# Kernel tuning notes

Measured on AMD Instinct MI355X. Metric: run time of the kernel, lower is better.

The kernel has to match this reference:

```python
import jax, jax.numpy as jnp
import numpy as np

N = 100000      # nodes
R = 8           # relations
E_DIM = 128     # embedding dim
N_EDGES = 1600000  # n * avg_degree(16)


def setup_inputs() -> dict:
    key = jax.random.key(0)
    k1, k2, k3, k4, k5 = jax.random.split(key, 5)
    x = jax.random.normal(k1, (N, E_DIM), dtype=jnp.float32)
    # xavier-ish scale for (r, e, e) relation weights
    weights = jax.random.normal(k2, (R, E_DIM, E_DIM), dtype=jnp.float32) * (1.0 / np.sqrt(E_DIM))
    edge_rel = jax.random.randint(k3, (N_EDGES,), 0, R, dtype=jnp.int32)
    edge_src = jax.random.randint(k4, (N_EDGES,), 0, N, dtype=jnp.int32)
    edge_dst = jax.random.randint(k5, (N_EDGES,), 0, N, dtype=jnp.int32)
    return dict(x=x, weights=weights, edge_rel=edge_rel, edge_src=edge_src, edge_dst=edge_dst)


def reference(x, weights, edge_rel, edge_src, edge_dst):
    n, e = x.shape
    r = weights.shape[0]
    # sparse adjacency row index: relation-block row = rel * n + dst  (shape rn)
    rows = edge_rel.astype(jnp.int32) * n + edge_dst.astype(jnp.int32)
    # row-normalized values: vals = 1 / row_degree (util.sum_sparse)
    deg = jax.ops.segment_sum(jnp.ones(rows.shape, dtype=x.dtype), rows, num_segments=r * n)
    vals = 1.0 / deg[rows]  # only evaluated at rows with >=1 edge
    # SpMM: h = graph @ x, viewed as (r, n, e)
    msgs = vals[:, None] * x[edge_src]                       # (E, e) gather
    h = jax.ops.segment_sum(msgs, rows, num_segments=r * n)  # (r*n, e) scatter-add
    h = h.reshape(r, n, e)
    # per-relation transform: (r, e_out, e_in) x (r, n, e_in) -> (n, r, e_out)
    h = jnp.einsum('rih,rnh->nri', weights, h)
    # SumUnify: relu(sum over relations)
    return jax.nn.relu(h.sum(axis=1))
```

## Files before the change

### kernel.cpp

```cpp
#include <hip/hip_runtime.h>
#include <hip/hip_bf16.h>

#define ED 128
#define RR 8
#define KTOT (RR * ED)
#define LDB 136

typedef __attribute__((ext_vector_type(8))) short short8;
typedef __attribute__((ext_vector_type(4))) float f32x4;

__device__ __forceinline__ unsigned short f2bf(float f){
  unsigned int u = __builtin_bit_cast(unsigned int, f);
  return (unsigned short)((u + 0x7fffu + ((u >> 16) & 1u)) >> 16);
}
__device__ __forceinline__ float bf2f(unsigned int lo){
  return __builtin_bit_cast(float, lo << 16);
}

__global__ void cast_bf16_vec(const float4* __restrict__ in, ushort4* __restrict__ out, int n4){
  int stride = gridDim.x * blockDim.x;
  for (int i = blockIdx.x * blockDim.x + threadIdx.x; i < n4; i += stride){
    float4 v = in[i];
    ushort4 o;
    o.x = f2bf(v.x); o.y = f2bf(v.y); o.z = f2bf(v.z); o.w = f2bf(v.w);
    out[i] = o;
  }
}

__global__ void hist_rank(const int* __restrict__ rel, const int* __restrict__ dst,
                          int* __restrict__ rowcnt, int* __restrict__ rank, int E){
  int stride = gridDim.x * blockDim.x;
  for (int i = blockIdx.x * blockDim.x + threadIdx.x; i < E; i += stride)
    rank[i] = atomicAdd(&rowcnt[(dst[i] << 3) | rel[i]], 1);
}

__launch_bounds__(1024)
__global__ void scan_block_sum(const int* __restrict__ rowcnt, int* __restrict__ bsum, int m){
  __shared__ int lds[16];
  int t = threadIdx.x;
  int idx = blockIdx.x * 1024 + t;
  int v = (idx < m) ? rowcnt[idx] : 0;
#pragma unroll
  for (int o = 32; o > 0; o >>= 1) v += __shfl_down(v, o);
  if ((t & 63) == 0) lds[t >> 6] = v;
  __syncthreads();
  if (t == 0){
    int s = 0;
#pragma unroll
    for (int w = 0; w < 16; ++w) s += lds[w];
    bsum[blockIdx.x] = s;
  }
}

__launch_bounds__(1024)
__global__ void scan_bsum_par(const int* __restrict__ bsum, int* __restrict__ bscan,
                              int nb, int* __restrict__ total_out){
  __shared__ int wsum[16];
  int t = threadIdx.x, lane = t & 63, wid = t >> 6;
  int v = (t < nb) ? bsum[t] : 0;
  int incl = v;
#pragma unroll
  for (int o = 1; o < 64; o <<= 1){
    int u = __shfl_up(incl, o);
    if (lane >= o) incl += u;
  }
  if (lane == 63) wsum[wid] = incl;
  __syncthreads();
  int woff = 0;
  for (int w0 = 0; w0 < wid; ++w0) woff += wsum[w0];
  if (t < nb) bscan[t] = woff + incl - v;
  if (t == nb - 1) *total_out = woff + incl;
}

__launch_bounds__(1024)
__global__ void scan_final(const int* __restrict__ rowcnt, const int* __restrict__ bscan,
                           int* __restrict__ row_ptr, int m){
  __shared__ int wsum[16];
  int t = threadIdx.x, lane = t & 63, wid = t >> 6;
  int idx = blockIdx.x * 1024 + t;
  int v = (idx < m) ? rowcnt[idx] : 0;
  int incl = v;
#pragma unroll
  for (int o = 1; o < 64; o <<= 1){
    int u = __shfl_up(incl, o);
    if (lane >= o) incl += u;
  }
  if (lane == 63) wsum[wid] = incl;
  __syncthreads();
  int woff = bscan[blockIdx.x];
  for (int w0 = 0; w0 < wid; ++w0) woff += wsum[w0];
  if (idx < m) row_ptr[idx] = woff + incl - v;
}

__global__ void scatter_pos(const int* __restrict__ rel, const int* __restrict__ src,
                            const int* __restrict__ dst, const int* __restrict__ rank,
                            const int* __restrict__ row_ptr, int* __restrict__ payload, int E){
  int stride = gridDim.x * blockDim.x;
  for (int i = blockIdx.x * blockDim.x + threadIdx.x; i < E; i += stride){
    int key = (dst[i] << 3) | rel[i];
    payload[row_ptr[key] + rank[i]] = src[i];
  }
}

__launch_bounds__(256)
__global__ void row_agg(const unsigned short* __restrict__ xb,
                        const int* __restrict__ row_ptr8,
                        const int* __restrict__ payload,
                        unsigned short* __restrict__ h2, int n){
  int d = (blockIdx.x * 256 + threadIdx.x) >> 6;
  int lane = threadIdx.x & 63;
  if (d >= n) return;
  int p9 = 0;
  if (lane < 9) p9 = row_ptr8[(d << 3) + lane];
  int base = __builtin_amdgcn_readlane(p9, 0);
  int pl = payload[base + lane];
  int win = 0;
  unsigned int* hp = (unsigned int*)h2 + ((size_t)d << 9) + lane;
#pragma unroll
  for (int r = 0; r < RR; ++r){
    int beg = __builtin_amdgcn_readlane(p9, r);
    int end = __builtin_amdgcn_readlane(p9, r + 1);
    float ax = 0.f, ay = 0.f;
    for (int e = beg; e < end; ++e){
      int idx = e - base;
      if ((idx >> 6) != win){
        win = idx >> 6;
        pl = payload[base + (win << 6) + lane];
      }
      int s = __builtin_amdgcn_readlane(pl, idx & 63);
      unsigned int v = ((const unsigned int*)(xb + ((size_t)s << 7)))[lane];
      ax += bf2f(v & 0xffffu);
      ay += bf2f(v >> 16);
    }
    float sc = (end > beg) ? 1.f / (float)(end - beg) : 0.f;
    hp[r << 6] = ((unsigned int)f2bf(ay * sc) << 16) | f2bf(ax * sc);
  }
}

__launch_bounds__(256)
__global__ void gemm_out(const unsigned short* __restrict__ h2,
                         const unsigned short* __restrict__ wbb,
                         float* __restrict__ out, int n){
  __shared__ __align__(16) unsigned short lds_a[128 * LDB];
  __shared__ __align__(16) unsigned short lds_b[128 * LDB];
  const int t = threadIdx.x;
  const int wave = t >> 6, lane = t & 63;
  const int wr = wave >> 1, wc = wave & 1;
  const int dbase = blockIdx.x * 128;
  const int frow = lane & 15, kb = lane >> 4;

  f32x4 acc[4][4];
#pragma unroll
  for (int rt = 0; rt < 4; ++rt)
#pragma unroll
    for (int jt = 0; jt < 4; ++jt)
      acc[rt][jt] = (f32x4){0.f, 0.f, 0.f, 0.f};

  for (int r = 0; r < RR; ++r){
    __syncthreads();
#pragma unroll
    for (int p = 0; p < 8; ++p){
      int q = p * 256 + t;
      int row = q >> 4, col = q & 15;
      int gr = dbase + row; if (gr >= n) gr = n - 1;
      *(short8*)&lds_a[row * LDB + col * 8] =
          *(const short8*)(h2 + (size_t)gr * KTOT + r * ED + col * 8);
    }
    const unsigned short* wp = wbb + (size_t)r * ED * ED;
#pragma unroll
    for (int p = 0; p < 8; ++p){
      int q = p * 256 + t;
      int row = q >> 4, col = q & 15;
      *(short8*)&lds_b[row * LDB + col * 8] = *(const short8*)(wp + row * ED + col * 8);
    }
    __syncthreads();

    short8 a[4][4], b[4][4];
#pragma unroll
    for (int rt = 0; rt < 4; ++rt)
#pragma unroll
      for (int ks = 0; ks < 4; ++ks)
        a[rt][ks] = *(const short8*)&lds_a[(wr * 64 + rt * 16 + frow) * LDB + ks * 32 + kb * 8];
#pragma unroll
    for (int jt = 0; jt < 4; ++jt)
#pragma unroll
      for (int ks = 0; ks < 4; ++ks)
        b[jt][ks] = *(const short8*)&lds_b[(wc * 64 + jt * 16 + frow) * LDB + ks * 32 + kb * 8];
#pragma unroll
    for (int rt = 0; rt < 4; ++rt)
#pragma unroll
      for (int jt = 0; jt < 4; ++jt)
#pragma unroll
        for (int ks = 0; ks < 4; ++ks)
          acc[rt][jt] = __builtin_amdgcn_mfma_f32_16x16x32_bf16(a[rt][ks], b[jt][ks], acc[rt][jt], 0, 0, 0);
  }

  const int drow = (lane >> 4) * 4;
  const int dcol = lane & 15;
#pragma unroll
  for (int rt = 0; rt < 4; ++rt)
#pragma unroll
    for (int jt = 0; jt < 4; ++jt)
#pragma unroll
      for (int reg = 0; reg < 4; ++reg){
        int i = dbase + wr * 64 + rt * 16 + drow + reg;
        if (i < n)
          out[(size_t)i * ED + wc * 64 + jt * 16 + dcol] = fmaxf(acc[rt][jt][reg], 0.f);
      }
}

extern "C" void kernel_launch(void* const* d_in, const int* in_sizes, int n_in,
                              void* d_out, int out_size, void* d_ws, size_t ws_size,
                              hipStream_t stream){
  const float* x  = (const float*)d_in[0];
  const float* w  = (const float*)d_in[1];
  const int* erel = (const int*)d_in[2];
  const int* esrc = (const int*)d_in[3];
  const int* edst = (const int*)d_in[4];
  float* out = (float*)d_out;

  const int n = in_sizes[0] / ED;
  const int E = in_sizes[2];
  const int m = n * RR;
  const int NB = (m + 1023) / 1024;

  char* ws = (char*)d_ws;
  size_t off = 0;
  auto alloc = [&](size_t bytes) -> char* {
    char* p = ws + off;
    off += (bytes + 255) & ~(size_t)255;
    return p;
  };
  unsigned short* h2      = (unsigned short*)alloc((size_t)n * KTOT * 2);
  unsigned short* xb      = (unsigned short*)alloc((size_t)n * ED * 2);
  unsigned short* wbb     = (unsigned short*)alloc((size_t)RR * ED * ED * 2);
  int*            payload = (int*)alloc((size_t)E * 4);
  int*            row_ptr = (int*)alloc((size_t)(m + 1) * 4);
  int*            rowcnt  = (int*)alloc((size_t)m * 4);
  int*            rank    = (int*)alloc((size_t)E * 4);
  int*            bsum    = (int*)alloc((size_t)NB * 4);
  int*            bscan   = (int*)alloc((size_t)NB * 4);
  if (off > ws_size || NB > 1024) return;

  hipMemsetAsync(rowcnt, 0, (size_t)m * 4, stream);

  cast_bf16_vec<<<2048, 256, 0, stream>>>((const float4*)x, (ushort4*)xb, n * ED / 4);
  cast_bf16_vec<<<128, 256, 0, stream>>>((const float4*)w, (ushort4*)wbb, RR * ED * ED / 4);
  hist_rank    <<<2048, 256, 0, stream>>>(erel, edst, rowcnt, rank, E);
  scan_block_sum<<<NB, 1024, 0, stream>>>(rowcnt, bsum, m);
  scan_bsum_par<<<1, 1024, 0, stream>>>(bsum, bscan, NB, row_ptr + m);
  scan_final   <<<NB, 1024, 0, stream>>>(rowcnt, bscan, row_ptr, m);
  scatter_pos  <<<2048, 256, 0, stream>>>(erel, esrc, edst, rank, row_ptr, payload, E);
  row_agg      <<<(n + 3) / 4, 256, 0, stream>>>(xb, row_ptr, payload, h2, n);
  gemm_out     <<<(n + 127) / 128, 256, 0, stream>>>(h2, wbb, out, n);
}
```

Baseline: 336.1 us.

## Split row aggregation across four waves per node and unroll gathers by four

The row aggregation kernel now assigns four wavefronts per destination node, each handling two relations, rather than one wave doing all eight. Within a wave the edge loop issues up to four independent row gathers per iteration to raise memory-level parallelism, with a fallback path for segments longer than 64 edges. This targets latency-bound gather throughput but launches four times as many waves and duplicates row-pointer loads.

Result: faster. 319.2 us (-5.0%).

```diff
diff --git a/kernel.cpp b/kernel.cpp
--- a/kernel.cpp
+++ b/kernel.cpp
@@ -107,33 +107,69 @@
                         const int* __restrict__ row_ptr8,
                         const int* __restrict__ payload,
                         unsigned short* __restrict__ h2, int n){
-  int d = (blockIdx.x * 256 + threadIdx.x) >> 6;
+  int wv   = (blockIdx.x * 256 + threadIdx.x) >> 6;
   int lane = threadIdx.x & 63;
+  int d    = wv >> 2;
+  int half = wv & 3;
   if (d >= n) return;
-  int p9 = 0;
-  if (lane < 9) p9 = row_ptr8[(d << 3) + lane];
-  int base = __builtin_amdgcn_readlane(p9, 0);
-  int pl = payload[base + lane];
-  int win = 0;
-  unsigned int* hp = (unsigned int*)h2 + ((size_t)d << 9) + lane;
-#pragma unroll
-  for (int r = 0; r < RR; ++r){
-    int beg = __builtin_amdgcn_readlane(p9, r);
-    int end = __builtin_amdgcn_readlane(p9, r + 1);
-    float ax = 0.f, ay = 0.f;
-    for (int e = beg; e < end; ++e){
-      int idx = e - base;
-      if ((idx >> 6) != win){
-        win = idx >> 6;
-        pl = payload[base + (win << 6) + lane];
+
+  int p3 = 0;
+  if (lane < 3) p3 = row_ptr8[(d << 3) + (half << 1) + lane];
+  int b0 = __builtin_amdgcn_readlane(p3, 0);
+  int b1 = __builtin_amdgcn_readlane(p3, 1);
+  int b2 = __builtin_amdgcn_readlane(p3, 2);
+  unsigned int* hp = (unsigned int*)h2 + ((size_t)d << 9) + ((size_t)half << 7) + lane;
+
+  if (b2 - b0 <= 64){
+    int pl = payload[b0 + lane];
+#pragma unroll
+    for (int rr = 0; rr < 2; ++rr){
+      int beg = rr ? b1 : b0;
+      int end = rr ? b2 : b1;
+      float ax = 0.f, ay = 0.f;
+      for (int e = beg; e < end; e += 4){
+        int i0 = e - b0;
+        int i1 = (e + 1 < end ? e + 1 : end - 1) - b0;
+        int i2 = (e + 2 < end ? e + 2 : end - 1) - b0;
+        int i3 = (e + 3 < end ? e + 3 : end - 1) - b0;
+        unsigned int v0 = 0, v1 = 0, v2 = 0, v3 = 0;
+        int s0 = __builtin_amdgcn_readlane(pl, i0);
+        v0 = ((const unsigned int*)(xb + ((size_t)s0 << 7)))[lane];
+        if (e + 1 < end){
+          int s1 = __builtin_amdgcn_readlane(pl, i1);
+          v1 = ((const unsigned int*)(xb + ((size_t)s1 << 7)))[lane];
+        }
+        if (e + 2 < end){
+          int s2 = __builtin_amdgcn_readlane(pl, i2);
+          v2 = ((const unsigned int*)(xb + ((size_t)s2 << 7)))[lane];
+        }
+        if (e + 3 < end){
+          int s3 = __builtin_amdgcn_readlane(pl, i3);
+          v3 = ((const unsigned int*)(xb + ((size_t)s3 << 7)))[lane];
+        }
+        ax += bf2f(v0 & 0xffffu); ay += bf2f(v0 >> 16);
+        ax += bf2f(v1 & 0xffffu); ay += bf2f(v1 >> 16);
+        ax += bf2f(v2 & 0xffffu); ay += bf2f(v2 >> 16);
+        ax += bf2f(v3 & 0xffffu); ay += bf2f(v3 >> 16);
       }
-      int s = __builtin_amdgcn_readlane(pl, idx & 63);
-      unsigned int v = ((const unsigned int*)(xb + ((size_t)s << 7)))[lane];
-      ax += bf2f(v & 0xffffu);
-      ay += bf2f(v >> 16);
-    }
-    float sc = (end > beg) ? 1.f / (float)(end - beg) : 0.f;
-    hp[r << 6] = ((unsigned int)f2bf(ay * sc) << 16) | f2bf(ax * sc);
+      float sc = (end > beg) ? 1.f / (float)(end - beg) : 0.f;
+      hp[rr << 6] = ((unsigned int)f2bf(ay * sc) << 16) | f2bf(ax * sc);
+    }
+  } else {
+#pragma unroll
+    for (int rr = 0; rr < 2; ++rr){
+      int beg = rr ? b1 : b0;
+      int end = rr ? b2 : b1;
+      float ax = 0.f, ay = 0.f;
+      for (int e = beg; e < end; ++e){
+        int s = __builtin_amdgcn_readfirstlane(payload[e]);
+        unsigned int v = ((const unsigned int*)(xb + ((size_t)s << 7)))[lane];
+        ax += bf2f(v & 0xffffu);
+        ay += bf2f(v >> 16);
+      }
+      float sc = (end > beg) ? 1.f / (float)(end - beg) : 0.f;
+      hp[rr << 6] = ((unsigned int)f2bf(ay * sc) << 16) | f2bf(ax * sc);
+    }
   }
 }
 
@@ -251,6 +287,6 @@
   scan_bsum_par<<<1, 1024, 0, stream>>>(bsum, bscan, NB, row_ptr + m);
   scan_final   <<<NB, 1024, 0, stream>>>(rowcnt, bscan, row_ptr, m);
   scatter_pos  <<<2048, 256, 0, stream>>>(erel, esrc, edst, rank, row_ptr, payload, E);
-  row_agg      <<<(n + 3) / 4, 256, 0, stream>>>(xb, row_ptr, payload, h2, n);
+  row_agg      <<<(n * 4 + 3) / 4, 256, 0, stream>>>(xb, row_ptr, payload, h2, n);
   gemm_out     <<<(n + 127) / 128, 256, 0, stream>>>(h2, wbb, out, n);
 }
```

## Split row aggregation across two waves per node with unrolled flat edge loop

Applied to the files above, without the earlier changes.

Row aggregation now uses two waves per destination node, each covering four relations. Each wave walks its edges as one flat list, unrolled by four, and routes every gathered row to a per-relation accumulator. This exposes more parallelism and memory-level parallelism in the gather. It also removes the per-relation window reload logic. Nontemporal loads and stores are added to the cast, the h2 write/read and the output store to reduce cache pollution, at the cost of extra compare/select work per edge.

Measured after the change: 293.0 us. 12.8% less time.

```diff
diff --git a/kernel.cpp b/kernel.cpp
--- a/kernel.cpp
+++ b/kernel.cpp
@@ -8,6 +8,9 @@
 
 typedef __attribute__((ext_vector_type(8))) short short8;
 typedef __attribute__((ext_vector_type(4))) float f32x4;
+typedef __attribute__((ext_vector_type(4))) unsigned short u16x4;
+
+#define RL(v, i) __builtin_amdgcn_readlane(v, i)
 
 __device__ __forceinline__ unsigned short f2bf(float f){
   unsigned int u = __builtin_bit_cast(unsigned int, f);
@@ -16,14 +19,17 @@
 __device__ __forceinline__ float bf2f(unsigned int lo){
   return __builtin_bit_cast(float, lo << 16);
 }
-
-__global__ void cast_bf16_vec(const float4* __restrict__ in, ushort4* __restrict__ out, int n4){
+__device__ __forceinline__ unsigned int packbf(float hi, float lo){
+  return ((unsigned int)f2bf(hi) << 16) | f2bf(lo);
+}
+
+__global__ void cast_bf16_vec(const float* __restrict__ in, unsigned short* __restrict__ out, int n4){
   int stride = gridDim.x * blockDim.x;
   for (int i = blockIdx.x * blockDim.x + threadIdx.x; i < n4; i += stride){
-    float4 v = in[i];
-    ushort4 o;
-    o.x = f2bf(v.x); o.y = f2bf(v.y); o.z = f2bf(v.z); o.w = f2bf(v.w);
-    out[i] = o;
+    f32x4 v = __builtin_nontemporal_load((const f32x4*)(in + (size_t)i * 4));
+    u16x4 o;
+    o[0] = f2bf(v[0]); o[1] = f2bf(v[1]); o[2] = f2bf(v[2]); o[3] = f2bf(v[3]);
+    *(u16x4*)(out + (size_t)i * 4) = o;
   }
 }
 
@@ -107,34 +113,70 @@
                         const int* __restrict__ row_ptr8,
                         const int* __restrict__ payload,
                         unsigned short* __restrict__ h2, int n){
-  int d = (blockIdx.x * 256 + threadIdx.x) >> 6;
+  int wv   = (blockIdx.x * 256 + threadIdx.x) >> 6;
   int lane = threadIdx.x & 63;
+  int d    = wv >> 1;
+  int half = wv & 1;
   if (d >= n) return;
-  int p9 = 0;
-  if (lane < 9) p9 = row_ptr8[(d << 3) + lane];
-  int base = __builtin_amdgcn_readlane(p9, 0);
-  int pl = payload[base + lane];
-  int win = 0;
-  unsigned int* hp = (unsigned int*)h2 + ((size_t)d << 9) + lane;
-#pragma unroll
-  for (int r = 0; r < RR; ++r){
-    int beg = __builtin_amdgcn_readlane(p9, r);
-    int end = __builtin_amdgcn_readlane(p9, r + 1);
-    float ax = 0.f, ay = 0.f;
-    for (int e = beg; e < end; ++e){
-      int idx = e - base;
-      if ((idx >> 6) != win){
-        win = idx >> 6;
-        pl = payload[base + (win << 6) + lane];
-      }
-      int s = __builtin_amdgcn_readlane(pl, idx & 63);
+
+  int p5 = 0;
+  if (lane < 5) p5 = row_ptr8[(d << 3) + (half << 2) + lane];
+  int b0  = RL(p5, 0);
+  int o1  = RL(p5, 1) - b0;
+  int o2  = RL(p5, 2) - b0;
+  int o3  = RL(p5, 3) - b0;
+  int cnt = RL(p5, 4) - b0;
+
+  float ax0=0.f,ay0=0.f,ax1=0.f,ay1=0.f,ax2=0.f,ay2=0.f,ax3=0.f,ay3=0.f;
+
+#define ROUTE(VV, IDX) { \
+    float lo = bf2f((VV) & 0xffffu), hi = bf2f((VV) >> 16); \
+    if ((IDX) < o1)      { ax0 += lo; ay0 += hi; } \
+    else if ((IDX) < o2) { ax1 += lo; ay1 += hi; } \
+    else if ((IDX) < o3) { ax2 += lo; ay2 += hi; } \
+    else                 { ax3 += lo; ay3 += hi; } }
+
+  if (cnt <= 64){
+    int pl = payload[b0 + lane];
+    int e = 0;
+    for (; e + 4 <= cnt; e += 4){
+      int s0 = RL(pl, e);
+      int s1 = RL(pl, e + 1);
+      int s2 = RL(pl, e + 2);
+      int s3 = RL(pl, e + 3);
+      unsigned int v0 = ((const unsigned int*)(xb + ((size_t)s0 << 7)))[lane];
+      unsigned int v1 = ((const unsigned int*)(xb + ((size_t)s1 << 7)))[lane];
+      unsigned int v2 = ((const unsigned int*)(xb + ((size_t)s2 << 7)))[lane];
+      unsigned int v3 = ((const unsigned int*)(xb + ((size_t)s3 << 7)))[lane];
+      ROUTE(v0, e)
+      ROUTE(v1, e + 1)
+      ROUTE(v2, e + 2)
+      ROUTE(v3, e + 3)
+    }
+    for (; e < cnt; ++e){
+      int s = RL(pl, e);
       unsigned int v = ((const unsigned int*)(xb + ((size_t)s << 7)))[lane];
-      ax += bf2f(v & 0xffffu);
-      ay += bf2f(v >> 16);
-    }
-    float sc = (end > beg) ? 1.f / (float)(end - beg) : 0.f;
-    hp[r << 6] = ((unsigned int)f2bf(ay * sc) << 16) | f2bf(ax * sc);
-  }
+      ROUTE(v, e)
+    }
+  } else {
+    for (int e = 0; e < cnt; ++e){
+      int s = __builtin_amdgcn_readfirstlane(payload[b0 + e]);
+      unsigned int v = ((const unsigned int*)(xb + ((size_t)s << 7)))[lane];
+      ROUTE(v, e)
+    }
+  }
+#undef ROUTE
+
+  int d0 = o1, d1 = o2 - o1, d2 = o3 - o2, d3 = cnt - o3;
+  float s0f = d0 ? 1.f / (float)d0 : 0.f;
+  float s1f = d1 ? 1.f / (float)d1 : 0.f;
+  float s2f = d2 ? 1.f / (float)d2 : 0.f;
+  float s3f = d3 ? 1.f / (float)d3 : 0.f;
+  unsigned int* hp = (unsigned int*)h2 + ((size_t)d << 9) + (half << 8) + lane;
+  __builtin_nontemporal_store(packbf(ay0 * s0f, ax0 * s0f), hp);
+  __builtin_nontemporal_store(packbf(ay1 * s1f, ax1 * s1f), hp + 64);
+  __builtin_nontemporal_store(packbf(ay2 * s2f, ax2 * s2f), hp + 128);
+  __builtin_nontemporal_store(packbf(ay3 * s3f, ax3 * s3f), hp + 192);
 }
 
 __launch_bounds__(256)
@@ -163,8 +205,9 @@
       int q = p * 256 + t;
       int row = q >> 4, col = q & 15;
       int gr = dbase + row; if (gr >= n) gr = n - 1;
-      *(short8*)&lds_a[row * LDB + col * 8] =
-          *(const short8*)(h2 + (size_t)gr * KTOT + r * ED + col * 8);
+      short8 vv = __builtin_nontemporal_load(
+          (const short8*)(h2 + (size_t)gr * KTOT + r * ED + col * 8));
+      *(short8*)&lds_a[row * LDB + col * 8] = vv;
     }
     const unsigned short* wp = wbb + (size_t)r * ED * ED;
 #pragma unroll
@@ -205,7 +248,8 @@
       for (int reg = 0; reg < 4; ++reg){
         int i = dbase + wr * 64 + rt * 16 + drow + reg;
         if (i < n)
-          out[(size_t)i * ED + wc * 64 + jt * 16 + dcol] = fmaxf(acc[rt][jt][reg], 0.f);
+          __builtin_nontemporal_store(fmaxf(acc[rt][jt][reg], 0.f),
+                                      &out[(size_t)i * ED + wc * 64 + jt * 16 + dcol]);
       }
 }
 
@@ -242,15 +286,15 @@
   int*            bscan   = (int*)alloc((size_t)NB * 4);
   if (off > ws_size || NB > 1024) return;
 
-  hipMemsetAsync(rowcnt, 0, (size_t)m * 4, stream);
-
-  cast_bf16_vec<<<2048, 256, 0, stream>>>((const float4*)x, (ushort4*)xb, n * ED / 4);
-  cast_bf16_vec<<<128, 256, 0, stream>>>((const float4*)w, (ushort4*)wbb, RR * ED * ED / 4);
+  (void)hipMemsetAsync(rowcnt, 0, (size_t)m * 4, stream);
+
+  cast_bf16_vec<<<2048, 256, 0, stream>>>(x, xb, n * ED / 4);
+  cast_bf16_vec<<<128, 256, 0, stream>>>(w, wbb, RR * ED * ED / 4);
   hist_rank    <<<2048, 256, 0, stream>>>(erel, edst, rowcnt, rank, E);
   scan_block_sum<<<NB, 1024, 0, stream>>>(rowcnt, bsum, m);
   scan_bsum_par<<<1, 1024, 0, stream>>>(bsum, bscan, NB, row_ptr + m);
   scan_final   <<<NB, 1024, 0, stream>>>(rowcnt, bscan, row_ptr, m);
   scatter_pos  <<<2048, 256, 0, stream>>>(erel, esrc, edst, rank, row_ptr, payload, E);
-  row_agg      <<<(n + 3) / 4, 256, 0, stream>>>(xb, row_ptr, payload, h2, n);
+  row_agg      <<<(2 * n + 3) / 4, 256, 0, stream>>>(xb, row_ptr, payload, h2, n);
   gemm_out     <<<(n + 127) / 128, 256, 0, stream>>>(h2, wbb, out, n);
 }
```

## Fuse row aggregation into the relation GEMM, removing the h2 intermediate

Applied to the files above, without the earlier changes.

Row aggregation and the per-relation GEMM are merged into one kernel. Each 1024-thread block aggregates 128 destination nodes relation by relation, writes the normalized bf16 rows straight into LDS and runs MFMA on them, so the 200MB h2 buffer never goes to global memory. Each wave now processes 8 nodes at once with two edges per step, giving more independent gathers in flight. Nontemporal loads and stores are added to the cast and output paths. The cost is load imbalance, since every wave waits for its highest-degree node, plus a block-wide sync per relation and smaller MFMA tiles.

After: 374.4 us. 11.4% more time.

```diff
diff --git a/kernel.cpp b/kernel.cpp
--- a/kernel.cpp
+++ b/kernel.cpp
@@ -3,11 +3,13 @@
 
 #define ED 128
 #define RR 8
-#define KTOT (RR * ED)
 #define LDB 136
 
 typedef __attribute__((ext_vector_type(8))) short short8;
 typedef __attribute__((ext_vector_type(4))) float f32x4;
+typedef __attribute__((ext_vector_type(4))) unsigned short u16x4;
+
+#define RL(v, i) __builtin_amdgcn_readlane(v, i)
 
 __device__ __forceinline__ unsigned short f2bf(float f){
   unsigned int u = __builtin_bit_cast(unsigned int, f);
@@ -16,14 +18,17 @@
 __device__ __forceinline__ float bf2f(unsigned int lo){
   return __builtin_bit_cast(float, lo << 16);
 }
-
-__global__ void cast_bf16_vec(const float4* __restrict__ in, ushort4* __restrict__ out, int n4){
+__device__ __forceinline__ unsigned int packbf(float hi, float lo){
+  return ((unsigned int)f2bf(hi) << 16) | f2bf(lo);
+}
+
+__global__ void cast_bf16_vec(const float* __restrict__ in, unsigned short* __restrict__ out, int n4){
   int stride = gridDim.x * blockDim.x;
   for (int i = blockIdx.x * blockDim.x + threadIdx.x; i < n4; i += stride){
-    float4 v = in[i];
-    ushort4 o;
-    o.x = f2bf(v.x); o.y = f2bf(v.y); o.z = f2bf(v.z); o.w = f2bf(v.w);
-    out[i] = o;
+    f32x4 v = __builtin_nontemporal_load((const f32x4*)(in + (size_t)i * 4));
+    u16x4 o;
+    o[0] = f2bf(v[0]); o[1] = f2bf(v[1]); o[2] = f2bf(v[2]); o[3] = f2bf(v[3]);
+    *(u16x4*)(out + (size_t)i * 4) = o;
   }
 }
 
@@ -102,110 +107,118 @@
   }
 }
 
-__launch_bounds__(256)
-__global__ void row_agg(const unsigned short* __restrict__ xb,
-                        const int* __restrict__ row_ptr8,
-                        const int* __restrict__ payload,
-                        unsigned short* __restrict__ h2, int n){
-  int d = (blockIdx.x * 256 + threadIdx.x) >> 6;
-  int lane = threadIdx.x & 63;
-  if (d >= n) return;
-  int p9 = 0;
-  if (lane < 9) p9 = row_ptr8[(d << 3) + lane];
-  int base = __builtin_amdgcn_readlane(p9, 0);
-  int pl = payload[base + lane];
-  int win = 0;
-  unsigned int* hp = (unsigned int*)h2 + ((size_t)d << 9) + lane;
-#pragma unroll
-  for (int r = 0; r < RR; ++r){
-    int beg = __builtin_amdgcn_readlane(p9, r);
-    int end = __builtin_amdgcn_readlane(p9, r + 1);
-    float ax = 0.f, ay = 0.f;
-    for (int e = beg; e < end; ++e){
-      int idx = e - base;
-      if ((idx >> 6) != win){
-        win = idx >> 6;
-        pl = payload[base + (win << 6) + lane];
-      }
-      int s = __builtin_amdgcn_readlane(pl, idx & 63);
-      unsigned int v = ((const unsigned int*)(xb + ((size_t)s << 7)))[lane];
-      ax += bf2f(v & 0xffffu);
-      ay += bf2f(v >> 16);
-    }
-    float sc = (end > beg) ? 1.f / (float)(end - beg) : 0.f;
-    hp[r << 6] = ((unsigned int)f2bf(ay * sc) << 16) | f2bf(ax * sc);
-  }
-}
-
-__launch_bounds__(256)
-__global__ void gemm_out(const unsigned short* __restrict__ h2,
-                         const unsigned short* __restrict__ wbb,
-                         float* __restrict__ out, int n){
-  __shared__ __align__(16) unsigned short lds_a[128 * LDB];
+__launch_bounds__(1024, 8)
+__global__ void fused_agg_gemm(const unsigned short* __restrict__ xb,
+                               const unsigned short* __restrict__ wbb,
+                               const int* __restrict__ row_ptr8,
+                               const int* __restrict__ payload,
+                               float* __restrict__ out, int n, int m){
+  __shared__ __align__(16) unsigned short lds_h[128 * LDB];
   __shared__ __align__(16) unsigned short lds_b[128 * LDB];
   const int t = threadIdx.x;
   const int wave = t >> 6, lane = t & 63;
-  const int wr = wave >> 1, wc = wave & 1;
-  const int dbase = blockIdx.x * 128;
+  const int dbase = blockIdx.x << 7;
+  const int nb = dbase + (wave << 3);
   const int frow = lane & 15, kb = lane >> 4;
-
-  f32x4 acc[4][4];
-#pragma unroll
-  for (int rt = 0; rt < 4; ++rt)
-#pragma unroll
-    for (int jt = 0; jt < 4; ++jt)
+  const int mr = wave >> 2, nc = wave & 3;
+
+  int rowi = (nb << 3) + lane; if (rowi > m) rowi = m;
+  int pv = row_ptr8[rowi];
+  int rowe = (nb << 3) + 64; if (rowe > m) rowe = m;
+  int lastb = row_ptr8[rowe];
+  int wbase = RL(pv, 0);
+  int pl0 = payload[wbase + lane];
+  int pl1 = payload[wbase + 64 + lane];
+  int pl2 = payload[wbase + 128 + lane];
+
+  f32x4 acc[2][2];
+#pragma unroll
+  for (int rt = 0; rt < 2; ++rt)
+#pragma unroll
+    for (int jt = 0; jt < 2; ++jt)
       acc[rt][jt] = (f32x4){0.f, 0.f, 0.f, 0.f};
 
   for (int r = 0; r < RR; ++r){
+    int sg[8], dg[8];
+#pragma unroll
+    for (int i = 0; i < 8; ++i){
+      int bi = RL(pv, (i << 3) + r);
+      int ei = ((i << 3) + r + 1) < 64 ? RL(pv, (i << 3) + r + 1) : lastb;
+      sg[i] = bi - wbase;
+      dg[i] = ei - bi;
+    }
+    int dmax = dg[0];
+#pragma unroll
+    for (int i = 1; i < 8; ++i) dmax = dg[i] > dmax ? dg[i] : dmax;
+
+    float ax[8], ay[8];
+#pragma unroll
+    for (int i = 0; i < 8; ++i){ ax[i] = 0.f; ay[i] = 0.f; }
+
+#define SRC(IDX) ((IDX) < 64 ? RL(pl0, (IDX)) : (IDX) < 128 ? RL(pl1, (IDX) - 64) \
+                 : (IDX) < 192 ? RL(pl2, (IDX) - 128) : payload[wbase + (IDX)])
+
+    for (int j = 0; j < dmax; j += 2){
+      unsigned va[8], vb[8];
+#pragma unroll
+      for (int i = 0; i < 8; ++i){
+        if (j < dg[i]){
+          int s = SRC(sg[i] + j);
+          va[i] = ((const unsigned*)(xb + ((size_t)s << 7)))[lane];
+        }
+        if (j + 1 < dg[i]){
+          int s = SRC(sg[i] + j + 1);
+          vb[i] = ((const unsigned*)(xb + ((size_t)s << 7)))[lane];
+        }
+      }
+#pragma unroll
+      for (int i = 0; i < 8; ++i){
+        if (j < dg[i])    { ax[i] += bf2f(va[i] & 0xffffu); ay[i] += bf2f(va[i] >> 16); }
+        if (j + 1 < dg[i]){ ax[i] += bf2f(vb[i] & 0xffffu); ay[i] += bf2f(vb[i] >> 16); }
+      }
+    }
+#undef SRC
+
+    const unsigned short* wp = wbb + (r << 14);
+    const int brow = t >> 3, bcol = (t & 7) << 4;
+    short8 pb0 = *(const short8*)(wp + brow * ED + bcol);
+    short8 pb1 = *(const short8*)(wp + brow * ED + bcol + 8);
+
     __syncthreads();
 #pragma unroll
-    for (int p = 0; p < 8; ++p){
-      int q = p * 256 + t;
-      int row = q >> 4, col = q & 15;
-      int gr = dbase + row; if (gr >= n) gr = n - 1;
-      *(short8*)&lds_a[row * LDB + col * 8] =
-          *(const short8*)(h2 + (size_t)gr * KTOT + r * ED + col * 8);
-    }
-    const unsigned short* wp = wbb + (size_t)r * ED * ED;
-#pragma unroll
-    for (int p = 0; p < 8; ++p){
-      int q = p * 256 + t;
-      int row = q >> 4, col = q & 15;
-      *(short8*)&lds_b[row * LDB + col * 8] = *(const short8*)(wp + row * ED + col * 8);
-    }
+    for (int i = 0; i < 8; ++i){
+      float sc = dg[i] > 0 ? 1.f / (float)dg[i] : 0.f;
+      ((unsigned*)lds_h)[((wave << 3) + i) * (LDB / 2) + lane] = packbf(ay[i] * sc, ax[i] * sc);
+    }
+    *(short8*)&lds_b[brow * LDB + bcol] = pb0;
+    *(short8*)&lds_b[brow * LDB + bcol + 8] = pb1;
     __syncthreads();
 
-    short8 a[4][4], b[4][4];
-#pragma unroll
-    for (int rt = 0; rt < 4; ++rt)
-#pragma unroll
-      for (int ks = 0; ks < 4; ++ks)
-        a[rt][ks] = *(const short8*)&lds_a[(wr * 64 + rt * 16 + frow) * LDB + ks * 32 + kb * 8];
-#pragma unroll
-    for (int jt = 0; jt < 4; ++jt)
-#pragma unroll
-      for (int ks = 0; ks < 4; ++ks)
-        b[jt][ks] = *(const short8*)&lds_b[(wc * 64 + jt * 16 + frow) * LDB + ks * 32 + kb * 8];
-#pragma unroll
-    for (int rt = 0; rt < 4; ++rt)
-#pragma unroll
-      for (int jt = 0; jt < 4; ++jt)
-#pragma unroll
-        for (int ks = 0; ks < 4; ++ks)
-          acc[rt][jt] = __builtin_amdgcn_mfma_f32_16x16x32_bf16(a[rt][ks], b[jt][ks], acc[rt][jt], 0, 0, 0);
-  }
-
-  const int drow = (lane >> 4) * 4;
+#pragma unroll
+    for (int ks = 0; ks < 4; ++ks){
+      short8 a0 = *(const short8*)&lds_h[(mr * 32 + frow) * LDB + ks * 32 + kb * 8];
+      short8 a1 = *(const short8*)&lds_h[(mr * 32 + 16 + frow) * LDB + ks * 32 + kb * 8];
+      short8 b0 = *(const short8*)&lds_b[(nc * 32 + frow) * LDB + ks * 32 + kb * 8];
+      short8 b1 = *(const short8*)&lds_b[(nc * 32 + 16 + frow) * LDB + ks * 32 + kb * 8];
+      acc[0][0] = __builtin_amdgcn_mfma_f32_16x16x32_bf16(a0, b0, acc[0][0], 0, 0, 0);
+      acc[0][1] = __builtin_amdgcn_mfma_f32_16x16x32_bf16(a0, b1, acc[0][1], 0, 0, 0);
+      acc[1][0] = __builtin_amdgcn_mfma_f32_16x16x32_bf16(a1, b0, acc[1][0], 0, 0, 0);
+      acc[1][1] = __builtin_amdgcn_mfma_f32_16x16x32_bf16(a1, b1, acc[1][1], 0, 0, 0);
+    }
+  }
+
+  const int drow = (lane >> 4) << 2;
   const int dcol = lane & 15;
 #pragma unroll
-  for (int rt = 0; rt < 4; ++rt)
-#pragma unroll
-    for (int jt = 0; jt < 4; ++jt)
+  for (int rt = 0; rt < 2; ++rt)
+#pragma unroll
+    for (int jt = 0; jt < 2; ++jt)
 #pragma unroll
       for (int reg = 0; reg < 4; ++reg){
-        int i = dbase + wr * 64 + rt * 16 + drow + reg;
+        int i = dbase + mr * 32 + rt * 16 + drow + reg;
         if (i < n)
-          out[(size_t)i * ED + wc * 64 + jt * 16 + dcol] = fmaxf(acc[rt][jt][reg], 0.f);
+          __builtin_nontemporal_store(fmaxf(acc[rt][jt][reg], 0.f),
+                                      &out[(size_t)i * ED + nc * 32 + jt * 16 + dcol]);
       }
 }
 
@@ -231,7 +244,6 @@
     off += (bytes + 255) & ~(size_t)255;
     return p;
   };
-  unsigned short* h2      = (unsigned short*)alloc((size_t)n * KTOT * 2);
   unsigned short* xb      = (unsigned short*)alloc((size_t)n * ED * 2);
   unsigned short* wbb     = (unsigned short*)alloc((size_t)RR * ED * ED * 2);
   int*            payload = (int*)alloc((size_t)E * 4);
@@ -242,15 +254,14 @@
   int*            bscan   = (int*)alloc((size_t)NB * 4);
   if (off > ws_size || NB > 1024) return;
 
-  hipMemsetAsync(rowcnt, 0, (size_t)m * 4, stream);
-
-  cast_bf16_vec<<<2048, 256, 0, stream>>>((const float4*)x, (ushort4*)xb, n * ED / 4);
-  cast_bf16_vec<<<128, 256, 0, stream>>>((const float4*)w, (ushort4*)wbb, RR * ED * ED / 4);
+  (void)hipMemsetAsync(rowcnt, 0, (size_t)m * 4, stream);
+
+  cast_bf16_vec<<<2048, 256, 0, stream>>>(x, xb, n * ED / 4);
+  cast_bf16_vec<<<128, 256, 0, stream>>>(w, wbb, RR * ED * ED / 4);
   hist_rank    <<<2048, 256, 0, stream>>>(erel, edst, rowcnt, rank, E);
   scan_block_sum<<<NB, 1024, 0, stream>>>(rowcnt, bsum, m);
   scan_bsum_par<<<1, 1024, 0, stream>>>(bsum, bscan, NB, row_ptr + m);
   scan_final   <<<NB, 1024, 0, stream>>>(rowcnt, bscan, row_ptr, m);
   scatter_pos  <<<2048, 256, 0, stream>>>(erel, esrc, edst, rank, row_ptr, payload, E);
-  row_agg      <<<(n + 3) / 4, 256, 0, stream>>>(xb, row_ptr, payload, h2, n);
-  gemm_out     <<<(n + 127) / 128, 256, 0, stream>>>(h2, wbb, out, n);
-}
+  fused_agg_gemm<<<(n + 127) / 128, 1024, 0, stream>>>(xb, wbb, row_ptr, payload, out, n, m);
+}
```
